# Optimization experiments

Hardware: AMD Instinct MI355X
Metric: run time of the kernel (lower is better)

Reference implementation:

```python
import jax, jax.numpy as jnp
import numpy as np

B = 8192        # batch
OBS = 256       # obs_dim
ACT = 32        # action_dim -> output is 2*ACT (mu, log_std)
HID = 512       # hidden_dim
P = 8           # number of base policies (experts)
LOG_STD_MIN, LOG_STD_MAX = -5.0, 2.0


def setup_inputs() -> dict:
    key = jax.random.key(0)
    ks = jax.random.split(key, 14)
    s = 0.05
    return {
        "obs": jax.random.normal(ks[0], (B, OBS), dtype=jnp.float32),
        # gate network: obs -> HID -> HID -> P (softmax)
        "gw0": jax.random.normal(ks[1], (HID, OBS), dtype=jnp.float32) * s,
        "gb0": jnp.zeros((HID,), dtype=jnp.float32),
        "gw1": jax.random.normal(ks[2], (HID, HID), dtype=jnp.float32) * s,
        "gb1": jnp.zeros((HID,), dtype=jnp.float32),
        "gw2": jax.random.normal(ks[3], (P, HID), dtype=jnp.float32) * s,
        "gb2": jnp.zeros((P,), dtype=jnp.float32),
        # stacked expert (base-policy) trunk params, hidden_depth=2
        "ew0": jax.random.normal(ks[4], (P, HID, OBS), dtype=jnp.float32) * s,
        "eb0": jax.random.normal(ks[5], (P, HID), dtype=jnp.float32) * s,
        "ew1": jax.random.normal(ks[6], (P, HID, HID), dtype=jnp.float32) * s,
        "eb1": jax.random.normal(ks[7], (P, HID), dtype=jnp.float32) * s,
        "ew2": jax.random.normal(ks[8], (P, 2 * ACT, HID), dtype=jnp.float32) * s,
        "eb2": jax.random.normal(ks[9], (P, 2 * ACT), dtype=jnp.float32) * s,
    }


def _blend_linear(blend, W, b, x):
    # Math identical to: W_new = reshape(blend @ flatten(W,1)); bmm(W_new, x) + blend @ b
    # Contracted in the efficient order (per-expert GEMM then blend): [B,P,out] intermediate.
    y = jnp.einsum('bp,poi,bi->bo', blend, W, x, optimize=True)
    return y + blend @ b


def reference(obs, gw0, gb0, gw1, gb1, gw2, gb2, ew0, eb0, ew1, eb1, ew2, eb2):
    # gate network with softmax output
    h = jax.nn.relu(obs @ gw0.T + gb0)
    h = jax.nn.relu(h @ gw1.T + gb1)
    blend = jax.nn.softmax(h @ gw2.T + gb2, axis=-1)  # [B, P]

    # blended per-sample MLP (hidden_depth = 2)
    x = jax.nn.relu(_blend_linear(blend, ew0, eb0, obs))
    x = jax.nn.relu(_blend_linear(blend, ew1, eb1, x))
    x = _blend_linear(blend, ew2, eb2, x)  # [B, 2*ACT]

    mu, log_std = jnp.split(x, 2, axis=-1)
    log_std = jnp.tanh(log_std)
    log_std = LOG_STD_MIN + 0.5 * (LOG_STD_MAX - LOG_STD_MIN) * (log_std + 1.0)
    std = jnp.exp(log_std)
    # dist = SquashedNormal(mu, std); return its defining tensors
    return jnp.concatenate([mu, std], axis=-1)
```

## Files before the change

### kernel.cpp

```cpp
#include <hip/hip_runtime.h>
#include <hip/hip_bf16.h>
#include <cstdint>
#include <cstddef>

#define B_DIM   8192
#define OBS_DIM 256
#define ACT_DIM 32
#define HID_DIM 512
#define NEXPERT 8

typedef __attribute__((ext_vector_type(4))) float        f32x4;
typedef __attribute__((ext_vector_type(8))) short        s16x8;
typedef __attribute__((ext_vector_type(4))) unsigned int u32x4;

__device__ __forceinline__ unsigned cvt_pk_bf16(float lo, float hi) {
    unsigned r;
    asm("v_cvt_pk_bf16_f32 %0, %1, %2" : "=v"(r) : "v"(lo), "v"(hi));
    return r;
}
__device__ __forceinline__ float bf16_lo_f32(unsigned u) { return __uint_as_float(u << 16); }
__device__ __forceinline__ float bf16_hi_f32(unsigned u) { return __uint_as_float(u & 0xffff0000u); }

struct CvtArgs {
    const float*    s[7];
    unsigned short* d[7];
    int             nb[7];
};

__global__ __launch_bounds__(256) void cvt_multi(CvtArgs a) {
    int bid = blockIdx.x;
    int seg = 0, base = 0;
    while (seg < 6 && bid >= base + a.nb[seg]) { base += a.nb[seg]; ++seg; }
    int local = (bid - base) * 256 + threadIdx.x;
    const f32x4* s = (const f32x4*)a.s[seg];
    f32x4 v0 = s[local * 2 + 0];
    f32x4 v1 = s[local * 2 + 1];
    u32x4 o;
    o[0] = cvt_pk_bf16(v0[0], v0[1]);
    o[1] = cvt_pk_bf16(v0[2], v0[3]);
    o[2] = cvt_pk_bf16(v1[0], v1[1]);
    o[3] = cvt_pk_bf16(v1[2], v1[3]);
    ((u32x4*)a.d[seg])[local] = o;
}

__global__ __launch_bounds__(256) void gate_softmax(const unsigned short* __restrict__ h1,
                                                    const unsigned short* __restrict__ gw2,
                                                    const float* __restrict__ gb2,
                                                    float* __restrict__ blend) {
    const int lane = threadIdx.x & 63;
    const int wid  = threadIdx.x >> 6;
    const int row  = blockIdx.x * 4 + wid;

    u32x4 xv = *(const u32x4*)(h1 + (size_t)row * HID_DIM + lane * 8);
    float x[8];
#pragma unroll
    for (int j = 0; j < 4; ++j) {
        unsigned u   = xv[j];
        x[2 * j]     = bf16_lo_f32(u);
        x[2 * j + 1] = bf16_hi_f32(u);
    }
    float s[NEXPERT];
#pragma unroll
    for (int pp = 0; pp < NEXPERT; ++pp) {
        u32x4 wv = *(const u32x4*)(gw2 + (size_t)pp * HID_DIM + lane * 8);
        float d  = 0.f;
#pragma unroll
        for (int j = 0; j < 4; ++j) {
            unsigned u = wv[j];
            d += x[2 * j] * bf16_lo_f32(u);
            d += x[2 * j + 1] * bf16_hi_f32(u);
        }
        s[pp] = d;
    }
#pragma unroll
    for (int off = 1; off < 64; off <<= 1) {
#pragma unroll
        for (int pp = 0; pp < NEXPERT; ++pp) s[pp] += __shfl_xor(s[pp], off);
    }
    if (lane == 0) {
        float l[NEXPERT], m = -1e30f;
#pragma unroll
        for (int pp = 0; pp < NEXPERT; ++pp) { l[pp] = s[pp] + gb2[pp]; m = fmaxf(m, l[pp]); }
        float sum = 0.f;
#pragma unroll
        for (int pp = 0; pp < NEXPERT; ++pp) { l[pp] = __expf(l[pp] - m); sum += l[pp]; }
        float inv = 1.f / sum;
#pragma unroll
        for (int pp = 0; pp < NEXPERT; ++pp) blend[(size_t)row * NEXPERT + pp] = l[pp] * inv;
    }
}

template <int KIN, int NOUT>
__global__ __launch_bounds__(256, 2) void gemm_gate(const unsigned short* __restrict__ A,
                                                    const unsigned short* __restrict__ W,
                                                    const float* __restrict__ bias,
                                                    unsigned short* __restrict__ outb) {
    constexpr int BM = 128, BN = 64, BK = 64;

    __shared__ unsigned short sA[BM * BK];
    __shared__ unsigned short sB[BN * BK];

    const int t    = threadIdx.x;
    const int lane = t & 63;
    const int wid  = t >> 6;
    const int wm   = wid >> 1, wn = wid & 1;
    const int m0   = blockIdx.x * BM;
    const int n0   = blockIdx.y * BN;

    f32x4 acc[4][2];
#pragma unroll
    for (int i = 0; i < 4; ++i)
#pragma unroll
        for (int j = 0; j < 2; ++j) acc[i][j] = {0.f, 0.f, 0.f, 0.f};

#pragma unroll 1
    for (int kt = 0; kt < KIN / BK; ++kt) {
        const int ks = kt * BK;
        __syncthreads();
        const unsigned short* Wp = W + (size_t)n0 * KIN + ks;
#pragma unroll
        for (int c = 0; c < 2; ++c) {
            const int ch  = c * 256 + t;
            const int row = ch >> 3;
            const int gs  = (ch & 7) ^ (row & 7);
            __builtin_amdgcn_global_load_lds(
                (const __attribute__((address_space(1))) unsigned int*)(Wp + (size_t)row * KIN + gs * 8),
                (__attribute__((address_space(3))) unsigned int*)(sB + ch * 8), 16, 0, 0);
        }
        const unsigned short* Ap = A + (size_t)m0 * KIN + ks;
#pragma unroll
        for (int c = 0; c < 4; ++c) {
            const int ch  = c * 256 + t;
            const int row = ch >> 3;
            const int gs  = (ch & 7) ^ (row & 7);
            __builtin_amdgcn_global_load_lds(
                (const __attribute__((address_space(1))) unsigned int*)(Ap + (size_t)row * KIN + gs * 8),
                (__attribute__((address_space(3))) unsigned int*)(sA + ch * 8), 16, 0, 0);
        }
        __syncthreads();

#pragma unroll
        for (int kk = 0; kk < BK; kk += 32) {
            const int kb = kk + ((lane >> 4) << 3);
            s16x8 af[4], bfr[2];
#pragma unroll
            for (int mf = 0; mf < 4; ++mf) {
                const int row = wm * 64 + mf * 16 + (lane & 15);
                const int idx = (row * BK + kb) ^ ((row & 7) << 3);
                af[mf] = *(const s16x8*)(sA + idx);
            }
#pragma unroll
            for (int nf = 0; nf < 2; ++nf) {
                const int row = wn * 32 + nf * 16 + (lane & 15);
                const int idx = (row * BK + kb) ^ ((row & 7) << 3);
                bfr[nf] = *(const s16x8*)(sB + idx);
            }
#pragma unroll
            for (int mf = 0; mf < 4; ++mf)
#pragma unroll
                for (int nf = 0; nf < 2; ++nf)
                    acc[mf][nf] = __builtin_amdgcn_mfma_f32_16x16x32_bf16(af[mf], bfr[nf],
                                                                          acc[mf][nf], 0, 0, 0);
        }
    }

    const int cn = lane & 15;
    const int rb = (lane >> 4) << 2;
#pragma unroll
    for (int nf = 0; nf < 2; ++nf) {
        const int gn   = n0 + wn * 32 + nf * 16 + cn;
        const float bv = bias[gn];
#pragma unroll
        for (int mf = 0; mf < 4; ++mf) {
#pragma unroll
            for (int r = 0; r < 4; ++r) {
                const int gm = m0 + wm * 64 + mf * 16 + rb + r;
                float v = fmaxf(acc[mf][nf][r] + bv, 0.f);
                outb[(size_t)gm * NOUT + gn] = (unsigned short)(cvt_pk_bf16(v, v) & 0xffffu);
            }
        }
    }
}

template <int KIN, int NOUT, int BN, int KTILES>
__global__ __launch_bounds__(256, 2) void gemm_moe_sk(const unsigned short* __restrict__ A,
                                                      const unsigned short* __restrict__ W,
                                                      const float* __restrict__ blend,
                                                      float* __restrict__ part) {
    constexpr int BM = 128, BK = 64;
    constexpr int NF = BN / 32;

    __shared__ unsigned short sA[BM * BK];
    __shared__ unsigned short sB[BN * BK];

    const int t    = threadIdx.x;
    const int lane = t & 63;
    const int wid  = t >> 6;
    const int wm   = wid >> 1, wn = wid & 1;
    const int m0   = blockIdx.x * BM;
    const int n0   = blockIdx.y * BN;
    const int sp   = blockIdx.z;

    f32x4 acc[4][NF];
#pragma unroll
    for (int i = 0; i < 4; ++i)
#pragma unroll
        for (int j = 0; j < NF; ++j) acc[i][j] = {0.f, 0.f, 0.f, 0.f};

#pragma unroll 1
    for (int kt = 0; kt < KTILES; ++kt) {
        const int k0 = (sp * KTILES + kt) * BK;
        const int p  = k0 / KIN;
        const int ks = k0 % KIN;

        __syncthreads();
        const unsigned short* Wp = W + ((size_t)p * NOUT + n0) * KIN + ks;
#pragma unroll
        for (int c = 0; c < BN / 32; ++c) {
            const int ch  = c * 256 + t;
            const int row = ch >> 3;
            const int gs  = (ch & 7) ^ (row & 7);
            __builtin_amdgcn_global_load_lds(
                (const __attribute__((address_space(1))) unsigned int*)(Wp + (size_t)row * KIN + gs * 8),
                (__attribute__((address_space(3))) unsigned int*)(sB + ch * 8), 16, 0, 0);
        }
#pragma unroll
        for (int c = 0; c < 4; ++c) {
            const int ch  = c * 256 + t;
            const int row = ch >> 3;
            const int col = (ch & 7) << 3;
            const int gm  = m0 + row;
            u32x4 v = *(const u32x4*)(A + (size_t)gm * KIN + ks + col);
            const float sc = blend[(size_t)gm * NEXPERT + p];
#pragma unroll
            for (int q = 0; q < 4; ++q) {
                unsigned u = v[q];
                v[q] = cvt_pk_bf16(bf16_lo_f32(u) * sc, bf16_hi_f32(u) * sc);
            }
            const int idx = (row * BK + col) ^ ((row & 7) << 3);
            *(u32x4*)(sA + idx) = v;
        }
        __syncthreads();

#pragma unroll
        for (int kk = 0; kk < BK; kk += 32) {
            const int kb = kk + ((lane >> 4) << 3);
            s16x8 af[4], bfr[NF];
#pragma unroll
            for (int mf = 0; mf < 4; ++mf) {
                const int row = wm * 64 + mf * 16 + (lane & 15);
                const int idx = (row * BK + kb) ^ ((row & 7) << 3);
                af[mf] = *(const s16x8*)(sA + idx);
            }
#pragma unroll
            for (int nf = 0; nf < NF; ++nf) {
                const int row = wn * (BN / 2) + nf * 16 + (lane & 15);
                const int idx = (row * BK + kb) ^ ((row & 7) << 3);
                bfr[nf] = *(const s16x8*)(sB + idx);
            }
#pragma unroll
            for (int mf = 0; mf < 4; ++mf)
#pragma unroll
                for (int nf = 0; nf < NF; ++nf)
                    acc[mf][nf] = __builtin_amdgcn_mfma_f32_16x16x32_bf16(af[mf], bfr[nf],
                                                                          acc[mf][nf], 0, 0, 0);
        }
    }

    const int cn = lane & 15;
    const int rb = (lane >> 4) << 2;
    float* dst = part + (size_t)sp * B_DIM * NOUT;
#pragma unroll
    for (int mf = 0; mf < 4; ++mf) {
#pragma unroll
        for (int r = 0; r < 4; ++r) {
            const int gm = m0 + wm * 64 + mf * 16 + rb + r;
#pragma unroll
            for (int nf = 0; nf < NF; ++nf) {
                const int gn = n0 + wn * (BN / 2) + nf * 16 + cn;
                dst[(size_t)gm * NOUT + gn] = acc[mf][nf][r];
            }
        }
    }
}

__global__ __launch_bounds__(256) void reduce2_relu(const float* __restrict__ part,
                                                    const float* __restrict__ blend,
                                                    const float* __restrict__ eb,
                                                    unsigned short* __restrict__ out) {
    const int tid = blockIdx.x * 256 + threadIdx.x;
    const int row = tid >> 6;
    const int c0  = (tid & 63) << 3;

    const f32x4* p0 = (const f32x4*)(part + (size_t)row * HID_DIM + c0);
    const f32x4* p1 = (const f32x4*)(part + ((size_t)B_DIM + row) * HID_DIM + c0);
    f32x4 v0 = p0[0], v1 = p0[1], w0 = p1[0], w1 = p1[1];

    const f32x4* bl = (const f32x4*)(blend + (size_t)row * NEXPERT);
    const f32x4 b0 = bl[0], b1 = bl[1];
    const float blv[8] = {b0[0], b0[1], b0[2], b0[3], b1[0], b1[1], b1[2], b1[3]};

    float res[8];
#pragma unroll
    for (int j = 0; j < 4; ++j) { res[j] = v0[j] + w0[j]; res[4 + j] = v1[j] + w1[j]; }
#pragma unroll
    for (int pp = 0; pp < NEXPERT; ++pp) {
        const f32x4* e = (const f32x4*)(eb + (size_t)pp * HID_DIM + c0);
        const f32x4 e0 = e[0], e1 = e[1];
#pragma unroll
        for (int j = 0; j < 4; ++j) {
            res[j]     += blv[pp] * e0[j];
            res[4 + j] += blv[pp] * e1[j];
        }
    }
    u32x4 o;
#pragma unroll
    for (int j = 0; j < 4; ++j)
        o[j] = cvt_pk_bf16(fmaxf(res[2 * j], 0.f), fmaxf(res[2 * j + 1], 0.f));
    *(u32x4*)(out + (size_t)row * HID_DIM + c0) = o;
}

__global__ __launch_bounds__(256) void reduce8_head(const float* __restrict__ part,
                                                    const float* __restrict__ blend,
                                                    const float* __restrict__ eb2,
                                                    float* __restrict__ out) {
    const int tid = blockIdx.x * 256 + threadIdx.x;
    const int row = tid >> 3;
    const int c0  = (tid & 7) << 3;

    float res[8] = {0.f, 0.f, 0.f, 0.f, 0.f, 0.f, 0.f, 0.f};
#pragma unroll
    for (int sp = 0; sp < 8; ++sp) {
        const f32x4* ps = (const f32x4*)(part + ((size_t)sp * B_DIM + row) * 64 + c0);
        const f32x4 a = ps[0], b = ps[1];
#pragma unroll
        for (int j = 0; j < 4; ++j) { res[j] += a[j]; res[4 + j] += b[j]; }
    }
    const f32x4* bl = (const f32x4*)(blend + (size_t)row * NEXPERT);
    const f32x4 b0 = bl[0], b1 = bl[1];
    const float blv[8] = {b0[0], b0[1], b0[2], b0[3], b1[0], b1[1], b1[2], b1[3]};
#pragma unroll
    for (int pp = 0; pp < NEXPERT; ++pp) {
        const f32x4* e = (const f32x4*)(eb2 + (size_t)pp * 64 + c0);
        const f32x4 e0 = e[0], e1 = e[1];
#pragma unroll
        for (int j = 0; j < 4; ++j) {
            res[j]     += blv[pp] * e0[j];
            res[4 + j] += blv[pp] * e1[j];
        }
    }
    f32x4 o0, o1;
#pragma unroll
    for (int j = 0; j < 8; ++j) {
        const int col = c0 + j;
        float v = res[j];
        if (col >= ACT_DIM) {
            const float vc = fminf(fmaxf(v, -15.f), 15.f);
            const float e2 = __expf(2.f * vc);
            const float th = (e2 - 1.f) / (e2 + 1.f);
            v = __expf(-1.5f + 3.5f * th);
        }
        if (j < 4) o0[j] = v; else o1[j - 4] = v;
    }
    f32x4* dst = (f32x4*)(out + (size_t)row * 64 + c0);
    dst[0] = o0;
    dst[1] = o1;
}

extern "C" void kernel_launch(void* const* d_in, const int* in_sizes, int n_in,
                              void* d_out, int out_size, void* d_ws, size_t ws_size,
                              hipStream_t stream) {
    const float* obs = (const float*)d_in[0];
    const float* gw0 = (const float*)d_in[1];
    const float* gb0 = (const float*)d_in[2];
    const float* gw1 = (const float*)d_in[3];
    const float* gb1 = (const float*)d_in[4];
    const float* gw2 = (const float*)d_in[5];
    const float* gb2 = (const float*)d_in[6];
    const float* ew0 = (const float*)d_in[7];
    const float* eb0 = (const float*)d_in[8];
    const float* ew1 = (const float*)d_in[9];
    const float* eb1 = (const float*)d_in[10];
    const float* ew2 = (const float*)d_in[11];
    const float* eb2 = (const float*)d_in[12];

    char* w = (char*)d_ws;
    auto alloc = [&](size_t bytes) {
        char* r = w;
        w += (bytes + 255) & ~(size_t)255;
        return r;
    };
    unsigned short* obs_bf = (unsigned short*)alloc((size_t)B_DIM * OBS_DIM * 2);
    unsigned short* gw0_bf = (unsigned short*)alloc((size_t)HID_DIM * OBS_DIM * 2);
    unsigned short* gw1_bf = (unsigned short*)alloc((size_t)HID_DIM * HID_DIM * 2);
    unsigned short* gw2_bf = (unsigned short*)alloc((size_t)NEXPERT * HID_DIM * 2);
    unsigned short* ew0_bf = (unsigned short*)alloc((size_t)NEXPERT * HID_DIM * OBS_DIM * 2);
    unsigned short* ew1_bf = (unsigned short*)alloc((size_t)NEXPERT * HID_DIM * HID_DIM * 2);
    unsigned short* ew2_bf = (unsigned short*)alloc((size_t)NEXPERT * 2 * ACT_DIM * HID_DIM * 2);
    unsigned short* h0     = (unsigned short*)alloc((size_t)B_DIM * HID_DIM * 2);
    unsigned short* h1     = (unsigned short*)alloc((size_t)B_DIM * HID_DIM * 2);
    float*          blend  = (float*)alloc((size_t)B_DIM * NEXPERT * 4);
    float*          part   = (float*)alloc((size_t)2 * B_DIM * HID_DIM * 4);

    CvtArgs ca;
    ca.s[0] = obs; ca.d[0] = obs_bf; ca.nb[0] = (B_DIM * OBS_DIM / 8) / 256;
    ca.s[1] = gw0; ca.d[1] = gw0_bf; ca.nb[1] = (HID_DIM * OBS_DIM / 8) / 256;
    ca.s[2] = gw1; ca.d[2] = gw1_bf; ca.nb[2] = (HID_DIM * HID_DIM / 8) / 256;
    ca.s[3] = gw2; ca.d[3] = gw2_bf; ca.nb[3] = (NEXPERT * HID_DIM / 8) / 256;
    ca.s[4] = ew0; ca.d[4] = ew0_bf; ca.nb[4] = (NEXPERT * HID_DIM * OBS_DIM / 8) / 256;
    ca.s[5] = ew1; ca.d[5] = ew1_bf; ca.nb[5] = (NEXPERT * HID_DIM * HID_DIM / 8) / 256;
    ca.s[6] = ew2; ca.d[6] = ew2_bf; ca.nb[6] = (NEXPERT * 64 * HID_DIM / 8) / 256;
    int total_blocks = 0;
    for (int i = 0; i < 7; ++i) total_blocks += ca.nb[i];
    cvt_multi<<<total_blocks, 256, 0, stream>>>(ca);

    gemm_gate<OBS_DIM, HID_DIM><<<dim3(B_DIM / 128, HID_DIM / 64), 256, 0, stream>>>(
        obs_bf, gw0_bf, gb0, h0);
    gemm_gate<HID_DIM, HID_DIM><<<dim3(B_DIM / 128, HID_DIM / 64), 256, 0, stream>>>(
        h0, gw1_bf, gb1, h1);
    gate_softmax<<<B_DIM / 4, 256, 0, stream>>>(h1, gw2_bf, gb2, blend);

    gemm_moe_sk<OBS_DIM, HID_DIM, 128, 16><<<dim3(B_DIM / 128, HID_DIM / 128, 2), 256, 0, stream>>>(
        obs_bf, ew0_bf, blend, part);
    reduce2_relu<<<B_DIM * 64 / 256, 256, 0, stream>>>(part, blend, eb0, h0);

    gemm_moe_sk<HID_DIM, HID_DIM, 128, 32><<<dim3(B_DIM / 128, HID_DIM / 128, 2), 256, 0, stream>>>(
        h0, ew1_bf, blend, part);
    reduce2_relu<<<B_DIM * 64 / 256, 256, 0, stream>>>(part, blend, eb1, h1);

    gemm_moe_sk<HID_DIM, 64, 64, 8><<<dim3(B_DIM / 128, 1, 8), 256, 0, stream>>>(
        h1, ew2_bf, blend, part);
    reduce8_head<<<B_DIM * 8 / 256, 256, 0, stream>>>(part, blend, eb2, (float*)d_out);
}
```

Measured before the change: 224.5 us.

## Apply blend weights in epilogue per expert instead of scaling A tiles

Restructures the MoE split-K GEMM so each block loops over whole experts, accumulating an unscaled per-expert product in registers. The blend weight is applied to that accumulator once per expert. This removes the per-tile bf16 unpack/scale/repack of A and lets A be loaded directly to LDS via global_load_lds, the same path already used for the weights. In exchange it doubles the accumulator register footprint, which may reduce occupancy or cause spills, and it adds a small epilogue FMA per expert.

Result: faster. 214.8 us (-4.3%).

```diff
diff --git a/kernel.cpp b/kernel.cpp
--- a/kernel.cpp
+++ b/kernel.cpp
@@ -187,8 +187,11 @@
                                                       const unsigned short* __restrict__ W,
                                                       const float* __restrict__ blend,
                                                       float* __restrict__ part) {
-    constexpr int BM = 128, BK = 64;
-    constexpr int NF = BN / 32;
+    constexpr int BM   = 128, BK = 64;
+    constexpr int NF   = BN / 32;
+    constexpr int EXPT = KIN / BK;
+    constexpr int NPE  = KTILES / EXPT;
+    static_assert(KTILES % EXPT == 0, "split must align to expert boundary");
 
     __shared__ unsigned short sA[BM * BK];
     __shared__ unsigned short sB[BN * BK];
@@ -201,74 +204,89 @@
     const int n0   = blockIdx.y * BN;
     const int sp   = blockIdx.z;
 
-    f32x4 acc[4][NF];
-#pragma unroll
-    for (int i = 0; i < 4; ++i)
-#pragma unroll
-        for (int j = 0; j < NF; ++j) acc[i][j] = {0.f, 0.f, 0.f, 0.f};
-
-#pragma unroll 1
-    for (int kt = 0; kt < KTILES; ++kt) {
-        const int k0 = (sp * KTILES + kt) * BK;
-        const int p  = k0 / KIN;
-        const int ks = k0 % KIN;
-
-        __syncthreads();
-        const unsigned short* Wp = W + ((size_t)p * NOUT + n0) * KIN + ks;
-#pragma unroll
-        for (int c = 0; c < BN / 32; ++c) {
-            const int ch  = c * 256 + t;
-            const int row = ch >> 3;
-            const int gs  = (ch & 7) ^ (row & 7);
-            __builtin_amdgcn_global_load_lds(
-                (const __attribute__((address_space(1))) unsigned int*)(Wp + (size_t)row * KIN + gs * 8),
-                (__attribute__((address_space(3))) unsigned int*)(sB + ch * 8), 16, 0, 0);
-        }
-#pragma unroll
-        for (int c = 0; c < 4; ++c) {
-            const int ch  = c * 256 + t;
-            const int row = ch >> 3;
-            const int col = (ch & 7) << 3;
-            const int gm  = m0 + row;
-            u32x4 v = *(const u32x4*)(A + (size_t)gm * KIN + ks + col);
-            const float sc = blend[(size_t)gm * NEXPERT + p];
-#pragma unroll
-            for (int q = 0; q < 4; ++q) {
-                unsigned u = v[q];
-                v[q] = cvt_pk_bf16(bf16_lo_f32(u) * sc, bf16_hi_f32(u) * sc);
-            }
-            const int idx = (row * BK + col) ^ ((row & 7) << 3);
-            *(u32x4*)(sA + idx) = v;
-        }
-        __syncthreads();
-
-#pragma unroll
-        for (int kk = 0; kk < BK; kk += 32) {
-            const int kb = kk + ((lane >> 4) << 3);
-            s16x8 af[4], bfr[NF];
-#pragma unroll
-            for (int mf = 0; mf < 4; ++mf) {
-                const int row = wm * 64 + mf * 16 + (lane & 15);
-                const int idx = (row * BK + kb) ^ ((row & 7) << 3);
-                af[mf] = *(const s16x8*)(sA + idx);
-            }
-#pragma unroll
-            for (int nf = 0; nf < NF; ++nf) {
-                const int row = wn * (BN / 2) + nf * 16 + (lane & 15);
-                const int idx = (row * BK + kb) ^ ((row & 7) << 3);
-                bfr[nf] = *(const s16x8*)(sB + idx);
-            }
-#pragma unroll
-            for (int mf = 0; mf < 4; ++mf)
-#pragma unroll
-                for (int nf = 0; nf < NF; ++nf)
-                    acc[mf][nf] = __builtin_amdgcn_mfma_f32_16x16x32_bf16(af[mf], bfr[nf],
-                                                                          acc[mf][nf], 0, 0, 0);
-        }
-    }
-
     const int cn = lane & 15;
     const int rb = (lane >> 4) << 2;
+
+    f32x4 mast[4][NF];
+#pragma unroll
+    for (int i = 0; i < 4; ++i)
+#pragma unroll
+        for (int j = 0; j < NF; ++j) mast[i][j] = {0.f, 0.f, 0.f, 0.f};
+
+#pragma unroll 1
+    for (int pe = 0; pe < NPE; ++pe) {
+        const int p = sp * NPE + pe;
+        f32x4 eacc[4][NF];
+#pragma unroll
+        for (int i = 0; i < 4; ++i)
+#pragma unroll
+            for (int j = 0; j < NF; ++j) eacc[i][j] = {0.f, 0.f, 0.f, 0.f};
+
+        const unsigned short* Ap0 = A + (size_t)m0 * KIN;
+        const unsigned short* Wp0 = W + ((size_t)p * NOUT + n0) * KIN;
+
+#pragma unroll 1
+        for (int kt = 0; kt < EXPT; ++kt) {
+            const int ks = kt * BK;
+            __syncthreads();
+#pragma unroll
+            for (int c = 0; c < NF; ++c) {
+                const int ch  = c * 256 + t;
+                const int row = ch >> 3;
+                const int gs  = (ch & 7) ^ (row & 7);
+                __builtin_amdgcn_global_load_lds(
+                    (const __attribute__((address_space(1))) unsigned int*)(Wp0 + (size_t)row * KIN + ks + gs * 8),
+                    (__attribute__((address_space(3))) unsigned int*)(sB + ch * 8), 16, 0, 0);
+            }
+#pragma unroll
+            for (int c = 0; c < 4; ++c) {
+                const int ch  = c * 256 + t;
+                const int row = ch >> 3;
+                const int gs  = (ch & 7) ^ (row & 7);
+                __builtin_amdgcn_global_load_lds(
+                    (const __attribute__((address_space(1))) unsigned int*)(Ap0 + (size_t)row * KIN + ks + gs * 8),
+                    (__attribute__((address_space(3))) unsigned int*)(sA + ch * 8), 16, 0, 0);
+            }
+            __syncthreads();
+
+#pragma unroll
+            for (int kk = 0; kk < BK; kk += 32) {
+                const int kb = kk + ((lane >> 4) << 3);
+                s16x8 af[4], bfr[NF];
+#pragma unroll
+                for (int mf = 0; mf < 4; ++mf) {
+                    const int row = wm * 64 + mf * 16 + (lane & 15);
+                    const int idx = (row * BK + kb) ^ ((row & 7) << 3);
+                    af[mf] = *(const s16x8*)(sA + idx);
+                }
+#pragma unroll
+                for (int nf = 0; nf < NF; ++nf) {
+                    const int row = wn * (BN / 2) + nf * 16 + (lane & 15);
+                    const int idx = (row * BK + kb) ^ ((row & 7) << 3);
+                    bfr[nf] = *(const s16x8*)(sB + idx);
+                }
+#pragma unroll
+                for (int mf = 0; mf < 4; ++mf)
+#pragma unroll
+                    for (int nf = 0; nf < NF; ++nf)
+                        eacc[mf][nf] = __builtin_amdgcn_mfma_f32_16x16x32_bf16(af[mf], bfr[nf],
+                                                                               eacc[mf][nf], 0, 0, 0);
+            }
+        }
+
+#pragma unroll
+        for (int mf = 0; mf < 4; ++mf) {
+#pragma unroll
+            for (int r = 0; r < 4; ++r) {
+                const int gm = m0 + wm * 64 + mf * 16 + rb + r;
+                const float bl = blend[(size_t)gm * NEXPERT + p];
+#pragma unroll
+                for (int nf = 0; nf < NF; ++nf)
+                    mast[mf][nf][r] += bl * eacc[mf][nf][r];
+            }
+        }
+    }
+
     float* dst = part + (size_t)sp * B_DIM * NOUT;
 #pragma unroll
     for (int mf = 0; mf < 4; ++mf) {
@@ -278,7 +296,7 @@
 #pragma unroll
             for (int nf = 0; nf < NF; ++nf) {
                 const int gn = n0 + wn * (BN / 2) + nf * 16 + cn;
-                dst[(size_t)gm * NOUT + gn] = acc[mf][nf][r];
+                dst[(size_t)gm * NOUT + gn] = mast[mf][nf][r];
             }
         }
     }
```
